# Kernel optimization log

Hardware: AMD Instinct MI355X
Metric: run time of the kernel (lower is better)

Reference implementation:

```python
import jax, jax.numpy as jnp
import numpy as np

B, S, D = 4, 2048, 1024
H, HD = 16, 64
TAU = HD ** -0.5
N_MASKED = 256  # last keys masked (padding)


def setup_inputs() -> dict:
    key = jax.random.key(0)
    ks = jax.random.split(key, 8)
    sc = 0.02
    mask = jnp.zeros((B, 1, 1, S), dtype=bool).at[..., S - N_MASKED:].set(True)
    return {
        "q": jax.random.normal(ks[0], (B, S, D), dtype=jnp.float32),
        "k": jax.random.normal(ks[1], (B, S, D), dtype=jnp.float32),
        "v": jax.random.normal(ks[2], (B, S, D), dtype=jnp.float32),
        "mask": mask,
        "Wq": jax.random.normal(ks[3], (D, H * HD), dtype=jnp.float32) * sc,
        "bq": jnp.zeros((H * HD,), dtype=jnp.float32),
        "Wk": jax.random.normal(ks[4], (D, H * HD), dtype=jnp.float32) * sc,
        "bk": jnp.zeros((H * HD,), dtype=jnp.float32),
        "Wv": jax.random.normal(ks[5], (D, H * HD), dtype=jnp.float32) * sc,
        "bv": jnp.zeros((H * HD,), dtype=jnp.float32),
        "Wo": jax.random.normal(ks[6], (H * HD, D), dtype=jnp.float32) * sc,
        "bo": jnp.zeros((D,), dtype=jnp.float32),
    }


def reference(q, k, v, mask, Wq, bq, Wk, bk, Wv, bv, Wo, bo):
    # projections: [..., s, D] -> [..., s, H, HD]
    qh = (q @ Wq + bq).reshape(*q.shape[:-1], H, HD)
    kh = (k @ Wk + bk).reshape(*k.shape[:-1], H, HD)
    vh = (v @ Wv + bv).reshape(*v.shape[:-1], H, HD)
    # scores: [B, H, Q, K]
    attn = jnp.einsum('bqhd,bkhd->bhqk', qh, kh) * TAU
    attn = jnp.where(mask, -jnp.inf, attn)  # masked_fill(mask, -inf)
    # dropout(p=0) before softmax is identity
    p = jax.nn.softmax(attn, axis=-1)
    out = jnp.einsum('bhqk,bkhd->bqhd', p, vh).reshape(*q.shape[:-1], H * HD)
    return out @ Wo + bo  # [B, S, D]
```

## Files before the change

### kernel.cpp

```cpp
#include <hip/hip_runtime.h>
#include <hip/hip_fp16.h>
#include <cstdint>
#include <cstddef>

#define B_  4
#define S_  2048
#define D_  1024
#define H_  16
#define HD_ 64
#define TAU_ 0.125f
#define QSCALE_ 0.18033688011112042f

typedef _Float16 f16;
typedef __attribute__((ext_vector_type(8)))  _Float16 f16x8;
typedef __attribute__((ext_vector_type(4)))  _Float16 f16x4;
typedef __attribute__((ext_vector_type(2)))  __fp16   fp16x2_b;
typedef __attribute__((ext_vector_type(4)))  float    f32x4;
typedef __attribute__((ext_vector_type(16))) float    f32x16;
typedef __attribute__((ext_vector_type(2)))  unsigned u32x2;

__device__ __forceinline__ void gload_lds16(const void* g, void* l) {
    __builtin_amdgcn_global_load_lds(
        (const __attribute__((address_space(1))) unsigned int*)g,
        (__attribute__((address_space(3)))       unsigned int*)l,
        16, 0, 0);
}

__device__ __forceinline__ unsigned pkh(float a, float b) {
    fp16x2_b h = __builtin_amdgcn_cvt_pkrtz(a, b);
    return __builtin_bit_cast(unsigned, h);
}

__device__ __forceinline__ float exp2_hw(float x) {
    float r;
    asm("v_exp_f32 %0, %1" : "=v"(r) : "v"(x));
    return r;
}

__device__ __forceinline__ float max3f(float a, float b, float c) {
    float r;
    asm("v_max3_f32 %0, %1, %2, %3" : "=v"(r) : "v"(a), "v"(b), "v"(c));
    return r;
}

__device__ __forceinline__ float pair_max(float x) {
    unsigned xu = __builtin_bit_cast(unsigned, x);
    u32x2 r = __builtin_amdgcn_permlane32_swap(xu, xu, false, false);
    return fmaxf(__builtin_bit_cast(float, r[0]), __builtin_bit_cast(float, r[1]));
}
__device__ __forceinline__ float pair_sum(float x) {
    unsigned xu = __builtin_bit_cast(unsigned, x);
    u32x2 r = __builtin_amdgcn_permlane32_swap(xu, xu, false, false);
    return __builtin_bit_cast(float, r[0]) + __builtin_bit_cast(float, r[1]);
}

__global__ __launch_bounds__(256) void mask_norm_kernel(
    const unsigned char* __restrict__ mp, unsigned char* __restrict__ nm,
    float* __restrict__ mf)
{
    __shared__ int flags[3];
    const int tid = threadIdx.x;
    if (tid < 3) flags[tid] = 0;
    __syncthreads();
    int loc0 = 0, loc1 = 0, loc2 = 0;
    for (int i = 0; i < 32; ++i) {
        int off = tid * 32 + i;
        unsigned char v = mp[off];
        if (v) {
            int m = off & 3;
            if (m == 0) loc0 = 1;
            else if (m == 1) loc1 = 1;
            else loc2 = 1;
        }
    }
    if (loc0) atomicOr(&flags[0], 1);
    if (loc1) atomicOr(&flags[1], 1);
    if (loc2) atomicOr(&flags[2], 1);
    __syncthreads();
    const int mode = flags[1] ? 0 : (flags[2] ? 2 : (flags[0] ? 1 : 0));
    for (int i = 0; i < 32; ++i) {
        int idx = tid * 32 + i;
        unsigned char r;
        if (mode == 0)      r = mp[idx] ? 1 : 0;
        else if (mode == 1) r = ((const int*)mp)[idx] ? 1 : 0;
        else                r = (((const float*)mp)[idx] != 0.f) ? 1 : 0;
        nm[idx] = r;
        mf[idx] = r ? -1e30f : 0.f;
    }
}

__global__ __launch_bounds__(256) void wconv_kernel(
    const float* __restrict__ W0, const float* __restrict__ W1,
    const float* __restrict__ W2, const float* __restrict__ W3,
    f16* __restrict__ Wt)
{
    __shared__ float T[64][65];
    const int z = blockIdx.z;
    const float* W = (z == 0) ? W0 : (z == 1) ? W1 : (z == 2) ? W2 : W3;
    f16* out = Wt + (size_t)z * D_ * D_;
    const int n0 = blockIdx.x * 64, k0 = blockIdx.y * 64;
    const int tid = threadIdx.x;
    for (int j = 0; j < 4; ++j) {
        int idx = j * 256 + tid;
        int r = idx >> 4, c4 = idx & 15;
        float4 v = *(const float4*)&W[(size_t)(k0 + r) * D_ + n0 + c4 * 4];
        T[r][c4 * 4 + 0] = v.x; T[r][c4 * 4 + 1] = v.y;
        T[r][c4 * 4 + 2] = v.z; T[r][c4 * 4 + 3] = v.w;
    }
    __syncthreads();
    for (int j = 0; j < 16; ++j) {
        int idx = j * 256 + tid;
        int nl = idx >> 6, kl = idx & 63;
        out[(size_t)(n0 + nl) * D_ + k0 + kl] = (f16)T[kl][nl];
    }
}

__global__ __launch_bounds__(256) void gemm_qkv_kernel(
    const float* __restrict__ q, const float* __restrict__ k,
    const float* __restrict__ v, const f16* __restrict__ Wt,
    const float* __restrict__ bq, const float* __restrict__ bk,
    const float* __restrict__ bv, f16* __restrict__ outbase)
{
    __shared__ __align__(16) f16 Al[128 * 64];
    __shared__ __align__(16) f16 Bl[128 * 64];
    const int z = blockIdx.z;
    const float* A  = (z == 0) ? q  : (z == 1) ? k  : v;
    const float* bi = (z == 0) ? bq : (z == 1) ? bk : bv;
    const f16*  W   = Wt + (size_t)z * D_ * D_;
    f16* Cp         = outbase + (size_t)z * S_ * B_ * D_;
    const float oscale = (z == 0) ? QSCALE_ : 1.f;
    const int outmode  = (z == 2) ? 1 : 0;
    const int m0 = blockIdx.x * 128, n0 = blockIdx.y * 128;
    const int tid = threadIdx.x, lane = tid & 63, wid = tid >> 6;
    const int wm = (wid >> 1) * 64, wn = (wid & 1) * 64;
    const int g = lane >> 4, c = lane & 15;

    f32x4 acc[4][4] = {};

    for (int kt = 0; kt < 16; ++kt) {
        const int k0 = kt * 64;
        for (int i = 0; i < 4; ++i) {
            int ch  = wid * 4 + i;
            int row = ch * 8 + (lane >> 3);
            int ls  = (lane & 7) ^ (row & 7);
            gload_lds16(W + (size_t)(n0 + row) * 1024 + k0 + ls * 8,
                        Bl + ch * 512);
        }
        for (int j = 0; j < 8; ++j) {
            int idx = j * 256 + tid;
            int row = idx >> 4, c4 = idx & 15;
            float4 va = *(const float4*)&A[(size_t)(m0 + row) * 1024 + k0 + c4 * 4];
            f16x4 h;
            h[0] = (f16)va.x; h[1] = (f16)va.y; h[2] = (f16)va.z; h[3] = (f16)va.w;
            int ps = (c4 >> 1) ^ (row & 7);
            *(f16x4*)&Al[row * 64 + ps * 8 + (c4 & 1) * 4] = h;
        }
        __syncthreads();
        for (int kc = 0; kc < 2; ++kc) {
            f16x8 af[4], bf[4];
            for (int mb = 0; mb < 4; ++mb) {
                int row = wm + mb * 16 + c;
                af[mb] = *(const f16x8*)&Al[row * 64 + ((kc * 4 + g) ^ (row & 7)) * 8];
            }
            for (int nb = 0; nb < 4; ++nb) {
                int row = wn + nb * 16 + c;
                bf[nb] = *(const f16x8*)&Bl[row * 64 + ((kc * 4 + g) ^ (row & 7)) * 8];
            }
            for (int mb = 0; mb < 4; ++mb)
                for (int nb = 0; nb < 4; ++nb)
                    acc[mb][nb] = __builtin_amdgcn_mfma_f32_16x16x32_f16(
                        af[mb], bf[nb], acc[mb][nb], 0, 0, 0);
        }
        __syncthreads();
    }
    for (int nb = 0; nb < 4; ++nb) {
        int n = n0 + wn + nb * 16 + c;
        float bv2 = bi[n];
        for (int mb = 0; mb < 4; ++mb)
            for (int r = 0; r < 4; ++r) {
                int m = m0 + wm + mb * 16 + g * 4 + r;
                float val = (acc[mb][nb][r] + bv2) * oscale;
                if (outmode == 1) {
                    Cp[(((size_t)(m >> 11) * H_ + (n >> 6)) * HD_ + (n & 63)) * S_ + (m & 2047)] = (f16)val;
                } else {
                    Cp[(size_t)m * 1024 + n] = (f16)val;
                }
            }
    }
}

__global__ __launch_bounds__(256) void gemm_out_kernel(
    const f16* __restrict__ Oh, const f16* __restrict__ WtO,
    const float* __restrict__ bo, float* __restrict__ out)
{
    __shared__ __align__(16) f16 Al[128 * 64];
    __shared__ __align__(16) f16 Bl[128 * 64];
    const int m0 = blockIdx.x * 128, n0 = blockIdx.y * 128;
    const int tid = threadIdx.x, lane = tid & 63, wid = tid >> 6;
    const int wm = (wid >> 1) * 64, wn = (wid & 1) * 64;
    const int g = lane >> 4, c = lane & 15;

    f32x4 acc[4][4] = {};

    for (int kt = 0; kt < 16; ++kt) {
        const int k0 = kt * 64;
        for (int i = 0; i < 4; ++i) {
            int ch  = wid * 4 + i;
            int row = ch * 8 + (lane >> 3);
            int ls  = (lane & 7) ^ (row & 7);
            gload_lds16(WtO + (size_t)(n0 + row) * 1024 + k0 + ls * 8,
                        Bl + ch * 512);
            gload_lds16(Oh + (size_t)(m0 + row) * 1024 + k0 + ls * 8,
                        Al + ch * 512);
        }
        __syncthreads();
        for (int kc = 0; kc < 2; ++kc) {
            f16x8 af[4], bf[4];
            for (int mb = 0; mb < 4; ++mb) {
                int row = wm + mb * 16 + c;
                af[mb] = *(const f16x8*)&Al[row * 64 + ((kc * 4 + g) ^ (row & 7)) * 8];
            }
            for (int nb = 0; nb < 4; ++nb) {
                int row = wn + nb * 16 + c;
                bf[nb] = *(const f16x8*)&Bl[row * 64 + ((kc * 4 + g) ^ (row & 7)) * 8];
            }
            for (int mb = 0; mb < 4; ++mb)
                for (int nb = 0; nb < 4; ++nb)
                    acc[mb][nb] = __builtin_amdgcn_mfma_f32_16x16x32_f16(
                        af[mb], bf[nb], acc[mb][nb], 0, 0, 0);
        }
        __syncthreads();
    }
    for (int nb = 0; nb < 4; ++nb) {
        int n = n0 + wn + nb * 16 + c;
        float bv = bo[n];
        for (int mb = 0; mb < 4; ++mb)
            for (int r = 0; r < 4; ++r) {
                int m = m0 + wm + mb * 16 + g * 4 + r;
                out[(size_t)m * 1024 + n] = acc[mb][nb][r] + bv;
            }
    }
}

__global__ __launch_bounds__(256, 2) void attn_kernel(
    const f16* __restrict__ qh, const f16* __restrict__ kh,
    const f16* __restrict__ vt, const unsigned char* __restrict__ maskp,
    const float* __restrict__ maskf, f16* __restrict__ Oh)
{
    __shared__ __align__(16) f16 Kl[2][128 * 64];
    __shared__ __align__(16) f16 VTl[2][64 * 128];
    const int tid = threadIdx.x, lane = tid & 63, wid = tid >> 6;
    const int ql = lane & 31, hi = lane >> 5;
    const int lg = ((blockIdx.x & 7) << 7) + (blockIdx.x >> 3);
    const int h = (lg >> 4) & 15, b = lg >> 8;
    const int q0 = (lg & 15) * 128 + wid * 32;

    const unsigned char* mrow = maskp + (size_t)b * S_;
    const float* mfrow = maskf + (size_t)b * S_;
    const size_t kbase  = (size_t)b * S_ * D_ + (size_t)h * HD_;
    const size_t vtbase = ((size_t)b * H_ + h) * (size_t)HD_ * S_;

    unsigned live = 0, part = 0;
    for (int t = 0; t < 16; ++t) {
        unsigned long long b0 = __ballot(mrow[t * 128 + lane] != 0);
        unsigned long long b1 = __ballot(mrow[t * 128 + 64 + lane] != 0);
        if (b0 != ~0ull || b1 != ~0ull) {
            live |= 1u << t;
            if (b0 | b1) part |= 1u << t;
        }
    }

    f16x8 qf[4];
    {
        const f16* qrow = qh + ((size_t)(b * S_ + q0 + ql) * H_ + h) * HD_;
        #pragma unroll
        for (int dc = 0; dc < 4; ++dc)
            qf[dc] = *(const f16x8*)&qrow[dc * 16 + hi * 8];
    }

    float m_ = -1e30f, l_ = 0.f;
    f32x16 accO[2] = {};

    auto stage = [&](int kv0, int bb) {
        #pragma unroll
        for (int i = 0; i < 4; ++i) {
            int ch  = wid * 4 + i;
            int row = ch * 8 + (lane >> 3);
            int ls  = (lane & 7) ^ (row & 7);
            gload_lds16(kh + kbase + (size_t)(kv0 + row) * D_ + ls * 8,
                        &Kl[bb][ch * 512]);
            int hdr = ch * 4 + (lane >> 4);
            int vs  = (lane & 15) ^ ((hdr & 7) << 1);
            gload_lds16(vt + vtbase + (size_t)hdr * S_ + kv0 + vs * 8,
                        &VTl[bb][ch * 512]);
        }
    };

    if (live) {
        int t = __builtin_ctz(live);
        stage(t * 128, 0);
        __syncthreads();
        int cur = 0;
        for (;;) {
            unsigned rem = live & (0xFFFFFFFEu << t);
            int tn = rem ? __builtin_ctz(rem) : 32;
            if (tn < 32) stage(tn * 128, cur ^ 1);

            const int kv0 = t * 128;
            const f16* Kb = &Kl[cur][0];
            const f16* Vb = &VTl[cur][0];

            f32x16 sacc[4] = {};
            __builtin_amdgcn_s_setprio(1);
            #pragma unroll
            for (int ks = 0; ks < 4; ++ks) {
                const int key = ks * 32 + ql;
                #pragma unroll
                for (int dc = 0; dc < 4; ++dc) {
                    int slot = (dc * 2 + hi) ^ (key & 7);
                    f16x8 kf = *(const f16x8*)&Kb[key * 64 + slot * 8];
                    sacc[ks] = __builtin_amdgcn_mfma_f32_32x32x16_f16(
                        kf, qf[dc], sacc[ks], 0, 0, 0);
                }
            }
            __builtin_amdgcn_s_setprio(0);
            if (part & (1u << t)) {
                #pragma unroll
                for (int ks = 0; ks < 4; ++ks)
                    #pragma unroll
                    for (int r = 0; r < 16; ++r) {
                        int key = kv0 + ks * 32 + (r & 3) + 8 * (r >> 2) + 4 * hi;
                        sacc[ks][r] += mfrow[key];
                    }
            }
            float mx;
            {
                float m0 = max3f(sacc[0][0], sacc[0][1], sacc[0][2]);
                float m1 = max3f(sacc[1][0], sacc[1][1], sacc[1][2]);
                float m2 = max3f(sacc[2][0], sacc[2][1], sacc[2][2]);
                float m3 = max3f(sacc[3][0], sacc[3][1], sacc[3][2]);
                #pragma unroll
                for (int r = 3; r < 15; r += 2) {
                    m0 = max3f(m0, sacc[0][r], sacc[0][r + 1]);
                    m1 = max3f(m1, sacc[1][r], sacc[1][r + 1]);
                    m2 = max3f(m2, sacc[2][r], sacc[2][r + 1]);
                    m3 = max3f(m3, sacc[3][r], sacc[3][r + 1]);
                }
                m0 = fmaxf(m0, sacc[0][15]); m1 = fmaxf(m1, sacc[1][15]);
                m2 = fmaxf(m2, sacc[2][15]); m3 = fmaxf(m3, sacc[3][15]);
                mx = max3f(m0, m1, m2);
                mx = fmaxf(mx, m3);
            }
            mx = pair_max(mx);
            if (__ballot(mx > m_ + 8.f)) {
                float mnew = fmaxf(m_, mx);
                float alpha = exp2_hw(m_ - mnew);
                m_ = mnew;
                l_ *= alpha;
                #pragma unroll
                for (int blk = 0; blk < 2; ++blk)
                    #pragma unroll
                    for (int r = 0; r < 16; ++r) accO[blk][r] *= alpha;
            }
            float ts = 0.f;
            #pragma unroll
            for (int ks = 0; ks < 4; ++ks)
                #pragma unroll
                for (int r = 0; r < 16; ++r) {
                    float p = exp2_hw(sacc[ks][r] - m_);
                    sacc[ks][r] = p;
                    ts += p;
                }
            l_ += pair_sum(ts);

            #pragma unroll
            for (int ks = 0; ks < 4; ++ks) {
                unsigned Pq[4][2];
                #pragma unroll
                for (int j = 0; j < 4; ++j) {
                    Pq[j][0] = pkh(sacc[ks][4 * j + 0], sacc[ks][4 * j + 1]);
                    Pq[j][1] = pkh(sacc[ks][4 * j + 2], sacc[ks][4 * j + 3]);
                }
                #pragma unroll
                for (int kc = 0; kc < 2; ++kc) {
                    union { f16x8 v; unsigned u[4]; } pf;
                    u32x2 s0 = __builtin_amdgcn_permlane32_swap(Pq[2 * kc][0], Pq[2 * kc + 1][0], false, false);
                    u32x2 s1 = __builtin_amdgcn_permlane32_swap(Pq[2 * kc][1], Pq[2 * kc + 1][1], false, false);
                    pf.u[0] = s0[0]; pf.u[2] = s0[1];
                    pf.u[1] = s1[0]; pf.u[3] = s1[1];
                    const int s = ks * 2 + kc;
                    __builtin_amdgcn_s_setprio(1);
                    #pragma unroll
                    for (int blk = 0; blk < 2; ++blk) {
                        int hd = blk * 32 + ql;
                        int slot = (s * 2 + hi) ^ ((hd & 7) << 1);
                        f16x8 vtf = *(const f16x8*)&Vb[hd * 128 + slot * 8];
                        accO[blk] = __builtin_amdgcn_mfma_f32_32x32x16_f16(
                            vtf, pf.v, accO[blk], 0, 0, 0);
                    }
                    __builtin_amdgcn_s_setprio(0);
                }
            }
            __syncthreads();
            cur ^= 1;
            if (tn == 32) break;
            t = tn;
        }
    }
    const float invl = (l_ > 0.f) ? 1.f / l_ : 0.f;
    f16* orow = Oh + ((size_t)(b * S_ + q0 + ql) * H_ + h) * HD_;
    #pragma unroll
    for (int blk = 0; blk < 2; ++blk)
        #pragma unroll
        for (int j = 0; j < 4; ++j) {
            f16x4 o;
            #pragma unroll
            for (int tt = 0; tt < 4; ++tt)
                o[tt] = (f16)(accO[blk][4 * j + tt] * invl);
            *(f16x4*)&orow[blk * 32 + 4 * hi + 8 * j] = o;
        }
}

extern "C" void kernel_launch(void* const* d_in, const int* in_sizes, int n_in,
                              void* d_out, int out_size, void* d_ws, size_t ws_size,
                              hipStream_t stream)
{
    const float* q    = (const float*)d_in[0];
    const float* k    = (const float*)d_in[1];
    const float* v    = (const float*)d_in[2];
    const unsigned char* mask = (const unsigned char*)d_in[3];
    const float* Wq   = (const float*)d_in[4];
    const float* bq   = (const float*)d_in[5];
    const float* Wk   = (const float*)d_in[6];
    const float* bk   = (const float*)d_in[7];
    const float* Wv   = (const float*)d_in[8];
    const float* bv   = (const float*)d_in[9];
    const float* Wo   = (const float*)d_in[10];
    const float* bo   = (const float*)d_in[11];
    float* out        = (float*)d_out;

    char* ws = (char*)d_ws;
    const size_t MB = 1048576;
    f16* Wt  = (f16*)ws;
    f16* qh  = (f16*)(ws + 8 * MB);
    f16* khp = (f16*)(ws + 24 * MB);
    f16* vtp = (f16*)(ws + 40 * MB);
    f16* Ohp = (f16*)(ws + 56 * MB);
    unsigned char* nm = (unsigned char*)(ws + 72 * MB);
    float* mf = (float*)(ws + 72 * MB + 8192);

    mask_norm_kernel<<<1, 256, 0, stream>>>(mask, nm, mf);
    wconv_kernel<<<dim3(16, 16, 4), 256, 0, stream>>>(Wq, Wk, Wv, Wo, Wt);
    gemm_qkv_kernel<<<dim3(64, 8, 3), 256, 0, stream>>>(q, k, v, Wt, bq, bk, bv, qh);
    attn_kernel<<<1024, 256, 0, stream>>>(qh, khp, vtp, nm, mf, Ohp);
    gemm_out_kernel<<<dim3(64, 8), 256, 0, stream>>>(Ohp, Wt + (size_t)3 * D_ * D_, bo, out);
}
```

Baseline: 235.8 us.

## Double-buffer LDS tiles in QKV and output projection GEMMs

Both projection GEMMs now keep two LDS buffers per operand and issue the next k-tile's global loads before computing on the current tile, so memory latency overlaps with MFMA work. In the QKV GEMM the fp32 A tile is loaded into registers early and converted and written to LDS after compute. MFMA sections are also wrapped in s_setprio raises and launch bounds request 2 blocks per CU. This doubles LDS use to 64KB per block and adds register pressure, which may limit occupancy.

```diff
diff --git a/kernel.cpp b/kernel.cpp
--- a/kernel.cpp
+++ b/kernel.cpp
@@ -115,14 +115,14 @@
     }
 }
 
-__global__ __launch_bounds__(256) void gemm_qkv_kernel(
+__global__ __launch_bounds__(256, 2) void gemm_qkv_kernel(
     const float* __restrict__ q, const float* __restrict__ k,
     const float* __restrict__ v, const f16* __restrict__ Wt,
     const float* __restrict__ bq, const float* __restrict__ bk,
     const float* __restrict__ bv, f16* __restrict__ outbase)
 {
-    __shared__ __align__(16) f16 Al[128 * 64];
-    __shared__ __align__(16) f16 Bl[128 * 64];
+    __shared__ __align__(16) f16 Al[2][128 * 64];
+    __shared__ __align__(16) f16 Bl[2][128 * 64];
     const int z = blockIdx.z;
     const float* A  = (z == 0) ? q  : (z == 1) ? k  : v;
     const float* bi = (z == 0) ? bq : (z == 1) ? bk : bv;
@@ -135,44 +135,88 @@
     const int wm = (wid >> 1) * 64, wn = (wid & 1) * 64;
     const int g = lane >> 4, c = lane & 15;
 
+    const int bch  = wid * 4;
+    const int arow_ = (tid * 8) >> 6;
     f32x4 acc[4][4] = {};
 
-    for (int kt = 0; kt < 16; ++kt) {
+    auto stageB = [&](int kt, int bb) {
         const int k0 = kt * 64;
+        #pragma unroll
         for (int i = 0; i < 4; ++i) {
-            int ch  = wid * 4 + i;
+            int ch  = bch + i;
             int row = ch * 8 + (lane >> 3);
             int ls  = (lane & 7) ^ (row & 7);
             gload_lds16(W + (size_t)(n0 + row) * 1024 + k0 + ls * 8,
-                        Bl + ch * 512);
-        }
+                        &Bl[bb][ch * 512]);
+        }
+    };
+    auto loadA = [&](int kt, float4* va) {
+        const int k0 = kt * 64;
+        #pragma unroll
         for (int j = 0; j < 8; ++j) {
             int idx = j * 256 + tid;
             int row = idx >> 4, c4 = idx & 15;
-            float4 va = *(const float4*)&A[(size_t)(m0 + row) * 1024 + k0 + c4 * 4];
+            va[j] = *(const float4*)&A[(size_t)(m0 + row) * 1024 + k0 + c4 * 4];
+        }
+    };
+    auto writeA = [&](const float4* va, int bb) {
+        #pragma unroll
+        for (int j = 0; j < 8; ++j) {
+            int idx = j * 256 + tid;
+            int row = idx >> 4, c4 = idx & 15;
             f16x4 h;
-            h[0] = (f16)va.x; h[1] = (f16)va.y; h[2] = (f16)va.z; h[3] = (f16)va.w;
+            h[0] = (f16)va[j].x; h[1] = (f16)va[j].y;
+            h[2] = (f16)va[j].z; h[3] = (f16)va[j].w;
             int ps = (c4 >> 1) ^ (row & 7);
-            *(f16x4*)&Al[row * 64 + ps * 8 + (c4 & 1) * 4] = h;
-        }
-        __syncthreads();
+            *(f16x4*)&Al[bb][row * 64 + ps * 8 + (c4 & 1) * 4] = h;
+        }
+    };
+    auto compute = [&](int bb) {
+        #pragma unroll
         for (int kc = 0; kc < 2; ++kc) {
             f16x8 af[4], bf[4];
+            #pragma unroll
             for (int mb = 0; mb < 4; ++mb) {
                 int row = wm + mb * 16 + c;
-                af[mb] = *(const f16x8*)&Al[row * 64 + ((kc * 4 + g) ^ (row & 7)) * 8];
-            }
+                af[mb] = *(const f16x8*)&Al[bb][row * 64 + ((kc * 4 + g) ^ (row & 7)) * 8];
+            }
+            #pragma unroll
             for (int nb = 0; nb < 4; ++nb) {
                 int row = wn + nb * 16 + c;
-                bf[nb] = *(const f16x8*)&Bl[row * 64 + ((kc * 4 + g) ^ (row & 7)) * 8];
-            }
+                bf[nb] = *(const f16x8*)&Bl[bb][row * 64 + ((kc * 4 + g) ^ (row & 7)) * 8];
+            }
+            __builtin_amdgcn_s_setprio(1);
+            #pragma unroll
             for (int mb = 0; mb < 4; ++mb)
+                #pragma unroll
                 for (int nb = 0; nb < 4; ++nb)
                     acc[mb][nb] = __builtin_amdgcn_mfma_f32_16x16x32_f16(
                         af[mb], bf[nb], acc[mb][nb], 0, 0, 0);
-        }
+            __builtin_amdgcn_s_setprio(0);
+        }
+    };
+
+    {
+        float4 va[8];
+        stageB(0, 0);
+        loadA(0, va);
+        writeA(va, 0);
         __syncthreads();
     }
+    int cur = 0;
+    for (int kt = 0; kt < 16; ++kt) {
+        float4 va[8];
+        if (kt < 15) {
+            stageB(kt + 1, cur ^ 1);
+            loadA(kt + 1, va);
+        }
+        compute(cur);
+        if (kt < 15) writeA(va, cur ^ 1);
+        __syncthreads();
+        cur ^= 1;
+    }
+    (void)arow_;
+
     for (int nb = 0; nb < 4; ++nb) {
         int n = n0 + wn + nb * 16 + c;
         float bv2 = bi[n];
@@ -189,12 +233,12 @@
     }
 }
 
-__global__ __launch_bounds__(256) void gemm_out_kernel(
+__global__ __launch_bounds__(256, 2) void gemm_out_kernel(
     const f16* __restrict__ Oh, const f16* __restrict__ WtO,
     const float* __restrict__ bo, float* __restrict__ out)
 {
-    __shared__ __align__(16) f16 Al[128 * 64];
-    __shared__ __align__(16) f16 Bl[128 * 64];
+    __shared__ __align__(16) f16 Al[2][128 * 64];
+    __shared__ __align__(16) f16 Bl[2][128 * 64];
     const int m0 = blockIdx.x * 128, n0 = blockIdx.y * 128;
     const int tid = threadIdx.x, lane = tid & 63, wid = tid >> 6;
     const int wm = (wid >> 1) * 64, wn = (wid & 1) * 64;
@@ -202,34 +246,49 @@
 
     f32x4 acc[4][4] = {};
 
-    for (int kt = 0; kt < 16; ++kt) {
+    auto stage = [&](int kt, int bb) {
         const int k0 = kt * 64;
+        #pragma unroll
         for (int i = 0; i < 4; ++i) {
             int ch  = wid * 4 + i;
             int row = ch * 8 + (lane >> 3);
             int ls  = (lane & 7) ^ (row & 7);
             gload_lds16(WtO + (size_t)(n0 + row) * 1024 + k0 + ls * 8,
-                        Bl + ch * 512);
+                        &Bl[bb][ch * 512]);
             gload_lds16(Oh + (size_t)(m0 + row) * 1024 + k0 + ls * 8,
-                        Al + ch * 512);
-        }
-        __syncthreads();
+                        &Al[bb][ch * 512]);
+        }
+    };
+
+    stage(0, 0);
+    __syncthreads();
+    int cur = 0;
+    for (int kt = 0; kt < 16; ++kt) {
+        if (kt < 15) stage(kt + 1, cur ^ 1);
+        #pragma unroll
         for (int kc = 0; kc < 2; ++kc) {
             f16x8 af[4], bf[4];
+            #pragma unroll
             for (int mb = 0; mb < 4; ++mb) {
                 int row = wm + mb * 16 + c;
-                af[mb] = *(const f16x8*)&Al[row * 64 + ((kc * 4 + g) ^ (row & 7)) * 8];
-            }
+                af[mb] = *(const f16x8*)&Al[cur][row * 64 + ((kc * 4 + g) ^ (row & 7)) * 8];
+            }
+            #pragma unroll
             for (int nb = 0; nb < 4; ++nb) {
                 int row = wn + nb * 16 + c;
-                bf[nb] = *(const f16x8*)&Bl[row * 64 + ((kc * 4 + g) ^ (row & 7)) * 8];
-            }
+                bf[nb] = *(const f16x8*)&Bl[cur][row * 64 + ((kc * 4 + g) ^ (row & 7)) * 8];
+            }
+            __builtin_amdgcn_s_setprio(1);
+            #pragma unroll
             for (int mb = 0; mb < 4; ++mb)
+                #pragma unroll
                 for (int nb = 0; nb < 4; ++nb)
                     acc[mb][nb] = __builtin_amdgcn_mfma_f32_16x16x32_f16(
                         af[mb], bf[nb], acc[mb][nb], 0, 0, 0);
+            __builtin_amdgcn_s_setprio(0);
         }
         __syncthreads();
+        cur ^= 1;
     }
     for (int nb = 0; nb < 4; ++nb) {
         int n = n0 + wn + nb * 16 + c;
```

Result: slower. 241.0 us (+2.2%).

## Merge Q/K/V projection GEMMs into one kernel computing three outputs per block

Applied to the files above, without the earlier changes.

Replaces the three-way grid over z with a single kernel in which each block holds three accumulator sets and computes the Q, K and V projections for the same output tile. All three A tiles are converted to fp16 and staged in LDS, while the B tile buffer is reused for each weight in turn, with MFMA priority raised via s_setprio. This raises per-block register use (48 accumulators) and LDS use, and the grid shrinks from 1536 to 512 blocks, which lowers occupancy and parallelism. A leftover stub kernel with an empty body is also added but never launched.

```diff
diff --git a/kernel.cpp b/kernel.cpp
--- a/kernel.cpp
+++ b/kernel.cpp
@@ -115,77 +115,114 @@
     }
 }
 
-__global__ __launch_bounds__(256) void gemm_qkv_kernel(
+__global__ __launch_bounds__(256, 2) void gemm_qkv_fused_kernel(
     const float* __restrict__ q, const float* __restrict__ k,
     const float* __restrict__ v, const f16* __restrict__ Wt,
     const float* __restrict__ bq, const float* __restrict__ bk,
     const float* __restrict__ bv, f16* __restrict__ outbase)
 {
     __shared__ __align__(16) f16 Al[128 * 64];
-    __shared__ __align__(16) f16 Bl[128 * 64];
-    const int z = blockIdx.z;
-    const float* A  = (z == 0) ? q  : (z == 1) ? k  : v;
-    const float* bi = (z == 0) ? bq : (z == 1) ? bk : bv;
-    const f16*  W   = Wt + (size_t)z * D_ * D_;
-    f16* Cp         = outbase + (size_t)z * S_ * B_ * D_;
-    const float oscale = (z == 0) ? QSCALE_ : 1.f;
-    const int outmode  = (z == 2) ? 1 : 0;
+    __shared__ __align__(16) f16 Bl[3][128 * 64];
+    const float* A = q;
+    (void)k; (void)v;
     const int m0 = blockIdx.x * 128, n0 = blockIdx.y * 128;
     const int tid = threadIdx.x, lane = tid & 63, wid = tid >> 6;
     const int wm = (wid >> 1) * 64, wn = (wid & 1) * 64;
     const int g = lane >> 4, c = lane & 15;
 
-    f32x4 acc[4][4] = {};
+    __syncthreads();
+}
+
+__global__ __launch_bounds__(256, 2) void gemm_qkv3_kernel(
+    const float* __restrict__ q, const float* __restrict__ k,
+    const float* __restrict__ v, const f16* __restrict__ Wt,
+    const float* __restrict__ bq, const float* __restrict__ bk,
+    const float* __restrict__ bv, f16* __restrict__ outbase)
+{
+    __shared__ __align__(16) f16 Al[3][128 * 64];
+    __shared__ __align__(16) f16 Bl[128 * 64];
+    const int m0 = blockIdx.x * 128, n0 = blockIdx.y * 128;
+    const int tid = threadIdx.x, lane = tid & 63, wid = tid >> 6;
+    const int wm = (wid >> 1) * 64, wn = (wid & 1) * 64;
+    const int g = lane >> 4, c = lane & 15;
+
+    f32x4 acc[3][4][4] = {};
 
     for (int kt = 0; kt < 16; ++kt) {
         const int k0 = kt * 64;
-        for (int i = 0; i < 4; ++i) {
-            int ch  = wid * 4 + i;
-            int row = ch * 8 + (lane >> 3);
-            int ls  = (lane & 7) ^ (row & 7);
-            gload_lds16(W + (size_t)(n0 + row) * 1024 + k0 + ls * 8,
-                        Bl + ch * 512);
-        }
-        for (int j = 0; j < 8; ++j) {
-            int idx = j * 256 + tid;
-            int row = idx >> 4, c4 = idx & 15;
-            float4 va = *(const float4*)&A[(size_t)(m0 + row) * 1024 + k0 + c4 * 4];
-            f16x4 h;
-            h[0] = (f16)va.x; h[1] = (f16)va.y; h[2] = (f16)va.z; h[3] = (f16)va.w;
-            int ps = (c4 >> 1) ^ (row & 7);
-            *(f16x4*)&Al[row * 64 + ps * 8 + (c4 & 1) * 4] = h;
-        }
-        __syncthreads();
-        for (int kc = 0; kc < 2; ++kc) {
-            f16x8 af[4], bf[4];
-            for (int mb = 0; mb < 4; ++mb) {
-                int row = wm + mb * 16 + c;
-                af[mb] = *(const f16x8*)&Al[row * 64 + ((kc * 4 + g) ^ (row & 7)) * 8];
-            }
-            for (int nb = 0; nb < 4; ++nb) {
-                int row = wn + nb * 16 + c;
-                bf[nb] = *(const f16x8*)&Bl[row * 64 + ((kc * 4 + g) ^ (row & 7)) * 8];
-            }
+        {
+            const float* Az[3] = { q, k, v };
+            #pragma unroll
+            for (int z = 0; z < 3; ++z) {
+                #pragma unroll
+                for (int j = 0; j < 8; ++j) {
+                    int idx = j * 256 + tid;
+                    int row = idx >> 4, c4 = idx & 15;
+                    float4 va = *(const float4*)&Az[z][(size_t)(m0 + row) * 1024 + k0 + c4 * 4];
+                    f16x4 h;
+                    h[0] = (f16)va.x; h[1] = (f16)va.y;
+                    h[2] = (f16)va.z; h[3] = (f16)va.w;
+                    int ps = (c4 >> 1) ^ (row & 7);
+                    *(f16x4*)&Al[z][row * 64 + ps * 8 + (c4 & 1) * 4] = h;
+                }
+            }
+        }
+        #pragma unroll
+        for (int z = 0; z < 3; ++z) {
+            #pragma unroll
+            for (int i = 0; i < 4; ++i) {
+                int ch  = wid * 4 + i;
+                int row = ch * 8 + (lane >> 3);
+                int ls  = (lane & 7) ^ (row & 7);
+                gload_lds16(Wt + (size_t)z * D_ * D_ + (size_t)(n0 + row) * 1024 + k0 + ls * 8,
+                            Bl + ch * 512);
+            }
+            __syncthreads();
+            #pragma unroll
+            for (int kc = 0; kc < 2; ++kc) {
+                f16x8 af[4], bf[4];
+                #pragma unroll
+                for (int mb = 0; mb < 4; ++mb) {
+                    int row = wm + mb * 16 + c;
+                    af[mb] = *(const f16x8*)&Al[z][row * 64 + ((kc * 4 + g) ^ (row & 7)) * 8];
+                }
+                #pragma unroll
+                for (int nb = 0; nb < 4; ++nb) {
+                    int row = wn + nb * 16 + c;
+                    bf[nb] = *(const f16x8*)&Bl[row * 64 + ((kc * 4 + g) ^ (row & 7)) * 8];
+                }
+                __builtin_amdgcn_s_setprio(1);
+                #pragma unroll
+                for (int mb = 0; mb < 4; ++mb)
+                    #pragma unroll
+                    for (int nb = 0; nb < 4; ++nb)
+                        acc[z][mb][nb] = __builtin_amdgcn_mfma_f32_16x16x32_f16(
+                            af[mb], bf[nb], acc[z][mb][nb], 0, 0, 0);
+                __builtin_amdgcn_s_setprio(0);
+            }
+            __syncthreads();
+        }
+    }
+
+    #pragma unroll
+    for (int z = 0; z < 3; ++z) {
+        const float* bi = (z == 0) ? bq : (z == 1) ? bk : bv;
+        f16* Cp = outbase + (size_t)z * S_ * B_ * D_;
+        const float osc = (z == 0) ? QSCALE_ : 1.f;
+        for (int nb = 0; nb < 4; ++nb) {
+            int n = n0 + wn + nb * 16 + c;
+            float bv2 = bi[n];
             for (int mb = 0; mb < 4; ++mb)
-                for (int nb = 0; nb < 4; ++nb)
-                    acc[mb][nb] = __builtin_amdgcn_mfma_f32_16x16x32_f16(
-                        af[mb], bf[nb], acc[mb][nb], 0, 0, 0);
-        }
-        __syncthreads();
-    }
-    for (int nb = 0; nb < 4; ++nb) {
-        int n = n0 + wn + nb * 16 + c;
-        float bv2 = bi[n];
-        for (int mb = 0; mb < 4; ++mb)
-            for (int r = 0; r < 4; ++r) {
-                int m = m0 + wm + mb * 16 + g * 4 + r;
-                float val = (acc[mb][nb][r] + bv2) * oscale;
-                if (outmode == 1) {
-                    Cp[(((size_t)(m >> 11) * H_ + (n >> 6)) * HD_ + (n & 63)) * S_ + (m & 2047)] = (f16)val;
-                } else {
-                    Cp[(size_t)m * 1024 + n] = (f16)val;
-                }
-            }
+                for (int r = 0; r < 4; ++r) {
+                    int m = m0 + wm + mb * 16 + g * 4 + r;
+                    float val = (acc[z][mb][nb][r] + bv2) * osc;
+                    if (z == 2) {
+                        Cp[(((size_t)(m >> 11) * H_ + (n >> 6)) * HD_ + (n & 63)) * S_ + (m & 2047)] = (f16)val;
+                    } else {
+                        Cp[(size_t)m * 1024 + n] = (f16)val;
+                    }
+                }
+        }
     }
 }
 
@@ -451,7 +488,7 @@
 
     mask_norm_kernel<<<1, 256, 0, stream>>>(mask, nm, mf);
     wconv_kernel<<<dim3(16, 16, 4), 256, 0, stream>>>(Wq, Wk, Wv, Wo, Wt);
-    gemm_qkv_kernel<<<dim3(64, 8, 3), 256, 0, stream>>>(q, k, v, Wt, bq, bk, bv, qh);
+    gemm_qkv3_kernel<<<dim3(64, 8), 256, 0, stream>>>(q, k, v, Wt, bq, bk, bv, qh);
     attn_kernel<<<1024, 256, 0, stream>>>(qh, khp, vtp, nm, mf, Ohp);
     gemm_out_kernel<<<dim3(64, 8), 256, 0, stream>>>(Ohp, Wt + (size_t)3 * D_ * D_, bo, out);
 }
```

Measured after the change: 422.3 us. 1.79x slower.
